# Kernel optimization log

Hardware: AMD Instinct MI355X
Metric: run time of the kernel (lower is better)

The kernel has to match this reference:

```python
import jax, jax.numpy as jnp
import numpy as np

N_NODES = 50000
N_EDGES = 1600000
NODE_DIM = 128
EDGE_DIM = 64
HIDDEN = 128
K_HOPS = 2  # DGL TAGConv default k=2


def _uniform(key, shape, fan_in):
    bound = 1.0 / np.sqrt(fan_in)
    return jax.random.uniform(key, shape, jnp.float32, -bound, bound)


def setup_inputs() -> dict:
    key = jax.random.key(0)
    ks = jax.random.split(key, 12)
    d_msg_in = NODE_DIM + EDGE_DIM
    d_c1_in = (HIDDEN + NODE_DIM) * (K_HOPS + 1)
    d_c2_in = HIDDEN * (K_HOPS + 1)
    return {
        "node_fea": jax.random.normal(ks[0], (N_NODES, NODE_DIM), jnp.float32),
        "edge_fea": jax.random.normal(ks[1], (N_EDGES, EDGE_DIM), jnp.float32),
        "src": jax.random.randint(ks[2], (N_EDGES,), 0, N_NODES),
        "dst": jax.random.randint(ks[3], (N_EDGES,), 0, N_NODES),
        "msg_W": _uniform(ks[4], (d_msg_in, HIDDEN), d_msg_in),
        "msg_b": _uniform(ks[5], (HIDDEN,), d_msg_in),
        "W1": _uniform(ks[6], (d_c1_in, HIDDEN), d_c1_in),
        "b1": _uniform(ks[7], (HIDDEN,), d_c1_in),
        "W2": _uniform(ks[8], (d_c2_in, HIDDEN), d_c2_in),
        "b2": _uniform(ks[9], (HIDDEN,), d_c2_in),
        "Wp": _uniform(ks[10], (HIDDEN, 1), HIDDEN),
        "bp": _uniform(ks[11], (1,), HIDDEN),
    }


def reference(node_fea, edge_fea, src, dst, msg_W, msg_b, W1, b1, W2, b2, Wp, bp):
    n = node_fea.shape[0]
    # --- edge message: relu(Linear([src_fea, edge_fea])) then scatter-sum to dst ---
    msg = jax.nn.relu(jnp.concatenate([node_fea[src], edge_fea], axis=1) @ msg_W + msg_b)
    h_neigh = jax.ops.segment_sum(msg, dst, num_segments=n)  # [N, H]

    # --- TAGConv (k=2) symmetric in-degree normalization, DGL-style ---
    deg = jax.ops.segment_sum(jnp.ones((dst.shape[0],), node_fea.dtype), dst, num_segments=n)
    norm = jnp.maximum(deg, 1.0) ** -0.5  # [N]

    def prop(x):  # x: [N, D] -> norm * A^T (norm * x)
        return norm[:, None] * jax.ops.segment_sum((x * norm[:, None])[src], dst, num_segments=n)

    def tagconv(x, W, b):
        h1 = prop(x)
        h2 = prop(h1)
        return jnp.concatenate([x, h1, h2], axis=1) @ W + b

    h = jax.nn.relu(tagconv(jnp.concatenate([node_fea, h_neigh], axis=1), W1, b1))
    h = jax.nn.relu(tagconv(h, W2, b2))

    # --- dgl.mean_nodes (single graph) then predict ---
    hg = jnp.mean(h, axis=0)  # [H]
    return hg @ Wp + bp  # [1]
```

## Files before the change

kernel.cpp:

```cpp
#include <hip/hip_runtime.h>
#include <hip/hip_bf16.h>


typedef __attribute__((ext_vector_type(8))) short short8;
typedef __attribute__((ext_vector_type(4))) float f32x4;
typedef __attribute__((ext_vector_type(4))) unsigned u32x4;
typedef unsigned short ushort_t;

static __device__ __forceinline__ unsigned short f2bf(float x) {
  union { float f; unsigned u; } v{x};
  unsigned r = v.u + 0x7FFF + ((v.u >> 16) & 1);
  return (unsigned short)(r >> 16);
}
static __device__ __forceinline__ float bf2f(unsigned short h) {
  union { unsigned u; float f; } v{(unsigned)h << 16};
  return v.f;
}
static __device__ __forceinline__ float u2f(unsigned u) {
  union { unsigned u; float f; } v{u};
  return v.f;
}
static __device__ __forceinline__ unsigned cvtpk(float a, float b) {
  unsigned r;
  asm("v_cvt_pk_bf16_f32 %0, %1, %2" : "=v"(r) : "v"(a), "v"(b));
  return r;
}

__global__ void k_deg(const int* __restrict__ dst, int* __restrict__ deg, int E) {
  int i = blockIdx.x * blockDim.x + threadIdx.x;
  int stride = gridDim.x * blockDim.x;
  for (; i < E; i += stride) atomicAdd(&deg[dst[i]], 1);
}

__global__ void k_scan(const int* __restrict__ deg, float* __restrict__ norm,
                       int* __restrict__ offs, int* __restrict__ cursor, int N) {
  __shared__ int part[1024];
  const int t = threadIdx.x;
  const int C = (N + 1023) >> 10;
  const int b = t * C, e = min(b + C, N);
  int s = 0;
  for (int i = b; i < e; ++i) s += deg[i];
  part[t] = s;
  __syncthreads();
  for (int ofs = 1; ofs < 1024; ofs <<= 1) {
    int v = (t >= ofs) ? part[t - ofs] : 0;
    __syncthreads();
    part[t] += v;
    __syncthreads();
  }
  int base = (t == 0) ? 0 : part[t - 1];
  for (int i = b; i < e; ++i) {
    offs[i] = base;
    cursor[i] = base;
    int d = deg[i];
    base += d;
    norm[i] = rsqrtf((float)max(d, 1));
  }
  if (t == 0) offs[N] = part[1023];
}

__global__ void k_csr(const int* __restrict__ src, const int* __restrict__ dst,
                      int* __restrict__ cursor, int* __restrict__ csr_srcnode,
                      int* __restrict__ csr_eid, int* __restrict__ pos2node, int E) {
  int i = blockIdx.x * blockDim.x + threadIdx.x;
  int stride = gridDim.x * blockDim.x;
  for (; i < E; i += stride) {
    int d = dst[i];
    int pos = atomicAdd(&cursor[d], 1);
    csr_srcnode[pos] = src[i];
    csr_eid[pos] = i;
    pos2node[pos] = d;
  }
}

__global__ void k_prepW(const float* __restrict__ W, ushort_t* __restrict__ Wf_hi,
                        ushort_t* __restrict__ Wf_lo, int KC) {
  int id = blockIdx.x * 256 + threadIdx.x;
  if (id >= KC * 8192) return;
  int j = id & 7;
  int l = (id >> 3) & 63;
  int rest = id >> 9;
  int ks = rest & 1, nt = (rest >> 1) & 7, kc = rest >> 4;
  int k = kc * 64 + ks * 32 + (l >> 4) * 8 + j;
  int col = nt * 16 + (l & 15);
  float w = W[(size_t)k * 128 + col];
  unsigned short hi = f2bf(w);
  unsigned short lo = f2bf(w - bf2f(hi));
  Wf_hi[id] = hi;
  Wf_lo[id] = lo;
}

static __device__ __forceinline__ void stage_hilo(const float* base, int sq, int sr,
                                                  ushort_t* Xhi, ushort_t* Xlo) {
#pragma unroll
  for (int i2 = 0; i2 < 2; ++i2) {
    const int o = sq * 2 + i2;
    f32x4 a4 = *(const f32x4*)(base + sq * 16 + i2 * 8);
    f32x4 b4 = *(const f32x4*)(base + sq * 16 + i2 * 8 + 4);
    float x[8] = {a4[0], a4[1], a4[2], a4[3], b4[0], b4[1], b4[2], b4[3]};
    u32x4 vh, vl;
#pragma unroll
    for (int j = 0; j < 4; ++j) {
      unsigned hp = cvtpk(x[2 * j], x[2 * j + 1]);
      float h0 = u2f(hp << 16), h1 = u2f(hp & 0xffff0000u);
      vh[j] = hp;
      vl[j] = cvtpk(x[2 * j] - h0, x[2 * j + 1] - h1);
    }
    const int slot = (sr >> 4) * 128 + o * 16 + (sr & 15);
    *(u32x4*)(Xhi + (size_t)slot * 8) = vh;
    *(u32x4*)(Xlo + (size_t)slot * 8) = vl;
  }
}

__global__ __launch_bounds__(256) void k_mm(
    const float* __restrict__ A0, const ushort_t* __restrict__ Wf_hi,
    const ushort_t* __restrict__ Wf_lo, const float* __restrict__ bias,
    ushort_t* __restrict__ outZ, int M, int KC) {
  __shared__ __align__(16) char lds[49152];
  ushort_t* Xhi = (ushort_t*)lds;
  ushort_t* Xlo = (ushort_t*)(lds + 8192);
  ushort_t* Whi = (ushort_t*)(lds + 16384);
  ushort_t* Wlo = (ushort_t*)(lds + 32768);

  const int t = threadIdx.x;
  const int m0 = blockIdx.x * 64;
  const int l = t & 63, mt = t >> 6;
  const int sr = t & 63, sq = t >> 6;
  const int row = min(m0 + sr, M - 1);

  f32x4 acc[8];
#pragma unroll
  for (int nt = 0; nt < 8; ++nt) acc[nt] = (f32x4){0.f, 0.f, 0.f, 0.f};

  for (int kc = 0; kc < KC; ++kc) {
    __syncthreads();
    {
      const ulong2* gh = (const ulong2*)(Wf_hi + (size_t)kc * 8192);
      const ulong2* gl = (const ulong2*)(Wf_lo + (size_t)kc * 8192);
#pragma unroll
      for (int i = 0; i < 4; ++i) {
        ((ulong2*)Whi)[i * 256 + t] = gh[i * 256 + t];
        ((ulong2*)Wlo)[i * 256 + t] = gl[i * 256 + t];
      }
    }
    stage_hilo(A0 + (size_t)row * 128 + kc * 64, sq, sr, Xhi, Xlo);
    __syncthreads();
    const short8* Xh8 = (const short8*)Xhi;
    const short8* Xl8 = (const short8*)Xlo;
    const short8* Wh8 = (const short8*)Whi;
    const short8* Wl8 = (const short8*)Wlo;
#pragma unroll
    for (int ks = 0; ks < 2; ++ks) {
      short8 ah = Xh8[mt * 128 + ks * 64 + l];
      short8 al = Xl8[mt * 128 + ks * 64 + l];
#pragma unroll
      for (int nt = 0; nt < 8; ++nt) {
        short8 bh = Wh8[(nt * 2 + ks) * 64 + l];
        short8 bl = Wl8[(nt * 2 + ks) * 64 + l];
        acc[nt] = __builtin_amdgcn_mfma_f32_16x16x32_bf16(ah, bh, acc[nt], 0, 0, 0);
        acc[nt] = __builtin_amdgcn_mfma_f32_16x16x32_bf16(al, bh, acc[nt], 0, 0, 0);
        acc[nt] = __builtin_amdgcn_mfma_f32_16x16x32_bf16(ah, bl, acc[nt], 0, 0, 0);
      }
    }
  }
  const int l15 = l & 15, lh = l >> 4;
#pragma unroll
  for (int nt = 0; nt < 8; ++nt) {
    const int col = nt * 16 + l15;
#pragma unroll
    for (int rg = 0; rg < 4; ++rg) {
      const int r = m0 + mt * 16 + lh * 4 + rg;
      if (r < M) outZ[(size_t)r * 128 + col] = f2bf(acc[nt][rg] + bias[col]);
    }
  }
}

template <int BF16A>
__global__ __launch_bounds__(256) void k_mm3(
    const void* __restrict__ A0v, const float* __restrict__ A1, int split64,
    const ushort_t* __restrict__ Wf_hi, const ushort_t* __restrict__ Wf_lo,
    const float* __restrict__ rowscale, float* __restrict__ outA,
    ushort_t* __restrict__ outYB, ushort_t* __restrict__ outYC, int M, int KC) {
  __shared__ __align__(16) char lds[49152];
  ushort_t* Xhi = (ushort_t*)lds;
  ushort_t* Xlo = (ushort_t*)(lds + 8192);
  ushort_t* Whi = (ushort_t*)(lds + 16384);
  ushort_t* Wlo = (ushort_t*)(lds + 32768);

  const int t = threadIdx.x;
  const int m0 = blockIdx.x * 64;
  const int l = t & 63, mt = t >> 6;
  const int sr = t & 63, sq = t >> 6;
  const int row = min(m0 + sr, M - 1);

  f32x4 acc[3][8];
#pragma unroll
  for (int s = 0; s < 3; ++s)
#pragma unroll
    for (int nt = 0; nt < 8; ++nt) acc[s][nt] = (f32x4){0.f, 0.f, 0.f, 0.f};

  for (int kc = 0; kc < KC; ++kc) {
    __syncthreads();
    if constexpr (BF16A) {
      const ushort_t* base = (const ushort_t*)A0v + (size_t)row * 128 + kc * 64;
#pragma unroll
      for (int i2 = 0; i2 < 2; ++i2) {
        const int o = sq * 2 + i2;
        short8 v = *(const short8*)(base + sq * 16 + i2 * 8);
        const int slot = (sr >> 4) * 128 + o * 16 + (sr & 15);
        *(short8*)(Xhi + (size_t)slot * 8) = v;
      }
    } else {
      const float* A0 = (const float*)A0v;
      const float* base = (kc < split64) ? (A0 + (size_t)row * 128 + kc * 64)
                                         : (A1 + (size_t)row * 128 + (kc - split64) * 64);
      stage_hilo(base, sq, sr, Xhi, Xlo);
    }
#pragma unroll
    for (int s = 0; s < 3; ++s) {
      if (s) __syncthreads();
      {
        const ulong2* gh = (const ulong2*)(Wf_hi + ((size_t)s * KC + kc) * 8192);
        const ulong2* gl = (const ulong2*)(Wf_lo + ((size_t)s * KC + kc) * 8192);
#pragma unroll
        for (int i = 0; i < 4; ++i) {
          ((ulong2*)Whi)[i * 256 + t] = gh[i * 256 + t];
          ((ulong2*)Wlo)[i * 256 + t] = gl[i * 256 + t];
        }
      }
      __syncthreads();
      const short8* Xh8 = (const short8*)Xhi;
      const short8* Xl8 = (const short8*)Xlo;
      const short8* Wh8 = (const short8*)Whi;
      const short8* Wl8 = (const short8*)Wlo;
#pragma unroll
      for (int ks = 0; ks < 2; ++ks) {
        short8 ah = Xh8[mt * 128 + ks * 64 + l];
        short8 al;
        if constexpr (!BF16A) al = Xl8[mt * 128 + ks * 64 + l];
#pragma unroll
        for (int nt = 0; nt < 8; ++nt) {
          short8 bh = Wh8[(nt * 2 + ks) * 64 + l];
          short8 bl = Wl8[(nt * 2 + ks) * 64 + l];
          acc[s][nt] = __builtin_amdgcn_mfma_f32_16x16x32_bf16(ah, bh, acc[s][nt], 0, 0, 0);
          if constexpr (!BF16A)
            acc[s][nt] = __builtin_amdgcn_mfma_f32_16x16x32_bf16(al, bh, acc[s][nt], 0, 0, 0);
          acc[s][nt] = __builtin_amdgcn_mfma_f32_16x16x32_bf16(ah, bl, acc[s][nt], 0, 0, 0);
        }
      }
    }
  }
  const int l15 = l & 15, lh = l >> 4;
#pragma unroll
  for (int rg = 0; rg < 4; ++rg) {
    const int r = m0 + mt * 16 + lh * 4 + rg;
    if (r < M) {
      const float rs = rowscale[r];
#pragma unroll
      for (int nt = 0; nt < 8; ++nt) {
        const int col = nt * 16 + l15;
        outA[(size_t)r * 128 + col] = acc[0][nt][rg];
        outYB[(size_t)r * 128 + col] = f2bf(acc[1][nt][rg] * rs);
        outYC[(size_t)r * 128 + col] = f2bf(acc[2][nt][rg] * rs);
      }
    }
  }
}

__global__ __launch_bounds__(512, 6) void k_edge(
    const float* __restrict__ ef, const int* __restrict__ csr_srcnode,
    const int* __restrict__ csr_eid, const int* __restrict__ pos2node,
    const ushort_t* __restrict__ WfB_hi, const ushort_t* __restrict__ WfB_lo,
    const ushort_t* __restrict__ Zb, float* __restrict__ h_neigh) {
  __shared__ __align__(16) char lds[49152];
  ushort_t* Xh = (ushort_t*)lds;
  ushort_t* Whi = (ushort_t*)(lds + 16384);
  ushort_t* Wlo = (ushort_t*)(lds + 32768);
  ushort_t* Cs = (ushort_t*)lds;
  int* sN = (int*)(lds + 32768);

  const int t = threadIdx.x;
  const int b0 = blockIdx.x * 128;
  const int l = t & 63, mt = t >> 6;
  const int col = t & 127, q = t >> 7;
  const int rbase = b0 + q * 32;

  unsigned zp[16];
#pragma unroll
  for (int i = 0; i < 16; ++i) {
    unsigned a = Zb[(size_t)csr_srcnode[rbase + 2 * i] * 128 + col];
    unsigned b = Zb[(size_t)csr_srcnode[rbase + 2 * i + 1] * 128 + col];
    zp[i] = a | (b << 16);
  }
  {
    const ulong2* gh = (const ulong2*)WfB_hi;
    const ulong2* gl = (const ulong2*)WfB_lo;
#pragma unroll
    for (int i = 0; i < 2; ++i) {
      ((ulong2*)Whi)[i * 512 + t] = gh[i * 512 + t];
      ((ulong2*)Wlo)[i * 512 + t] = gl[i * 512 + t];
    }
  }
  {
    const int row = t >> 2, part = t & 3;
    const int eid = csr_eid[b0 + row];
    const float* rowp = ef + (size_t)eid * 64 + part * 16;
#pragma unroll
    for (int i2 = 0; i2 < 2; ++i2) {
      const int o = part * 2 + i2;
      f32x4 a4 = __builtin_nontemporal_load((const f32x4*)(rowp + i2 * 8));
      f32x4 b4 = __builtin_nontemporal_load((const f32x4*)(rowp + i2 * 8 + 4));
      u32x4 vh;
      vh[0] = cvtpk(a4[0], a4[1]);
      vh[1] = cvtpk(a4[2], a4[3]);
      vh[2] = cvtpk(b4[0], b4[1]);
      vh[3] = cvtpk(b4[2], b4[3]);
      const int slot = (row >> 4) * 128 + o * 16 + (row & 15);
      *(u32x4*)(Xh + (size_t)slot * 8) = vh;
    }
  }
  __syncthreads();

  f32x4 acc[8];
#pragma unroll
  for (int nt = 0; nt < 8; ++nt) acc[nt] = (f32x4){0.f, 0.f, 0.f, 0.f};
  {
    const short8* Xh8 = (const short8*)Xh;
    const short8* Wh8 = (const short8*)Whi;
    const short8* Wl8 = (const short8*)Wlo;
#pragma unroll
    for (int ks = 0; ks < 2; ++ks) {
      short8 ah = Xh8[mt * 128 + ks * 64 + l];
#pragma unroll
      for (int nt = 0; nt < 8; ++nt) {
        short8 bh = Wh8[(nt * 2 + ks) * 64 + l];
        short8 bl = Wl8[(nt * 2 + ks) * 64 + l];
        acc[nt] = __builtin_amdgcn_mfma_f32_16x16x32_bf16(ah, bh, acc[nt], 0, 0, 0);
        acc[nt] = __builtin_amdgcn_mfma_f32_16x16x32_bf16(ah, bl, acc[nt], 0, 0, 0);
      }
    }
  }
  __syncthreads();
  if (t < 128) sN[t] = pos2node[b0 + t];
  const int l15 = l & 15, lh = l >> 4;
#pragma unroll
  for (int nt = 0; nt < 8; ++nt) {
#pragma unroll
    for (int rg = 0; rg < 4; ++rg) {
      const int row = mt * 16 + lh * 4 + rg;
      const int c = nt * 16 + l15;
      Cs[row * 128 + (c ^ (((row >> 2) & 3) << 4))] = f2bf(acc[nt][rg]);
    }
  }
  __syncthreads();
  {
    int node = sN[q * 32];
    float ssum = 0.f;
#pragma unroll
    for (int r = 0; r < 32; ++r) {
      const int rr = q * 32 + r;
      float cz = bf2f(Cs[rr * 128 + (col ^ (((rr >> 2) & 3) << 4))]);
      float zf = u2f((r & 1) ? (zp[r >> 1] & 0xffff0000u) : (zp[r >> 1] << 16));
      float v = fmaxf(cz + zf, 0.f);
      if (r == 0) {
        ssum = v;
      } else {
        int n2 = sN[rr];
        if (n2 == node) {
          ssum += v;
        } else {
          unsafeAtomicAdd(&h_neigh[(size_t)node * 128 + col], ssum);
          node = n2;
          ssum = v;
        }
      }
    }
    unsafeAtomicAdd(&h_neigh[(size_t)node * 128 + col], ssum);
  }
}

__global__ __launch_bounds__(256) void k_propA(
    const ushort_t* __restrict__ YCt, const ushort_t* __restrict__ YBt,
    const int* __restrict__ offs, const int* __restrict__ csr_src,
    const float* __restrict__ norm, ushort_t* __restrict__ Qt, int N) {
  const int v = blockIdx.x * 4 + (threadIdx.x >> 6);
  const int lane = threadIdx.x & 63;
  if (v >= N) return;
  const int b = offs[v], e = offs[v + 1];
  const unsigned* yc = (const unsigned*)YCt;
  float ax = 0.f, ay = 0.f;
#pragma unroll 4
  for (int i = b; i < e; ++i) {
    unsigned x = yc[(size_t)csr_src[i] * 64 + lane];
    ax += u2f(x << 16);
    ay += u2f(x & 0xffff0000u);
  }
  float n = norm[v];
  float n2 = n * n;
  unsigned yb = ((const unsigned*)YBt)[(size_t)v * 64 + lane];
  float qx = u2f(yb << 16) + n2 * ax;
  float qy = u2f(yb & 0xffff0000u) + n2 * ay;
  ((unsigned*)Qt)[(size_t)v * 64 + lane] = cvtpk(qx, qy);
}

__global__ __launch_bounds__(256) void k_propB(
    const ushort_t* __restrict__ Qt, const float* __restrict__ YA,
    const float* __restrict__ bias, const int* __restrict__ offs,
    const int* __restrict__ csr_src, const float* __restrict__ norm,
    ushort_t* __restrict__ H, int N) {
  const int v = blockIdx.x * 4 + (threadIdx.x >> 6);
  const int lane = threadIdx.x & 63;
  if (v >= N) return;
  const int b = offs[v], e = offs[v + 1];
  const unsigned* qp = (const unsigned*)Qt;
  float ax = 0.f, ay = 0.f;
#pragma unroll 4
  for (int i = b; i < e; ++i) {
    unsigned x = qp[(size_t)csr_src[i] * 64 + lane];
    ax += u2f(x << 16);
    ay += u2f(x & 0xffff0000u);
  }
  float n = norm[v];
  float2 ya = ((const float2*)YA)[(size_t)v * 64 + lane];
  float2 bb = ((const float2*)bias)[lane];
  float hx = fmaxf(ya.x + n * ax + bb.x, 0.f);
  float hy = fmaxf(ya.y + n * ay + bb.y, 0.f);
  ((unsigned*)H)[(size_t)v * 64 + lane] = cvtpk(hx, hy);
}

__global__ void k_colsum(const ushort_t* __restrict__ h, float* __restrict__ hg, int N) {
  const int t = threadIdx.x;
  const int per = (N + gridDim.x - 1) / gridDim.x;
  const int n0 = blockIdx.x * per, n1 = min(n0 + per, N);
  float s = 0.f;
  for (int n = n0; n < n1; ++n) s += bf2f(h[(size_t)n * 128 + t]);
  unsafeAtomicAdd(&hg[t], s);
}

__global__ void k_final(const float* __restrict__ hg, const float* __restrict__ Wp,
                        const float* __restrict__ bp, float* __restrict__ out,
                        float invN) {
  __shared__ float red[128];
  const int t = threadIdx.x;
  red[t] = hg[t] * invN * Wp[t];
  __syncthreads();
  for (int s = 64; s > 0; s >>= 1) {
    if (t < s) red[t] += red[t + s];
    __syncthreads();
  }
  if (t == 0) out[0] = red[0] + bp[0];
}

extern "C" void kernel_launch(void* const* d_in, const int* in_sizes, int n_in,
                              void* d_out, int out_size, void* d_ws, size_t ws_size,
                              hipStream_t stream) {
  const float* node_fea = (const float*)d_in[0];
  const float* edge_fea = (const float*)d_in[1];
  const int* src = (const int*)d_in[2];
  const int* dst = (const int*)d_in[3];
  const float* msg_W = (const float*)d_in[4];
  const float* msg_b = (const float*)d_in[5];
  const float* W1 = (const float*)d_in[6];
  const float* b1 = (const float*)d_in[7];
  const float* W2 = (const float*)d_in[8];
  const float* b2 = (const float*)d_in[9];
  const float* Wp = (const float*)d_in[10];
  const float* bp = (const float*)d_in[11];

  const int N = in_sizes[0] / 128;
  const int E = in_sizes[2];

  char* p = (char*)d_ws;
  auto alloc = [&](size_t bytes) {
    char* r = p;
    p += (bytes + 255) & ~(size_t)255;
    return r;
  };
  int* deg = (int*)alloc((size_t)N * 4);
  float* norm = (float*)alloc((size_t)N * 4);
  int* offs = (int*)alloc((size_t)(N + 1) * 4);
  int* cursor = (int*)alloc((size_t)N * 4);
  int* csr_srcnode = (int*)alloc((size_t)E * 4);
  int* csr_eid = (int*)alloc((size_t)E * 4);
  int* pos2node = (int*)alloc((size_t)E * 4);
  ushort_t* WfT_hi = (ushort_t*)alloc(2 * 8192 * 2);
  ushort_t* WfT_lo = (ushort_t*)alloc(2 * 8192 * 2);
  ushort_t* WfB_hi = (ushort_t*)alloc(1 * 8192 * 2);
  ushort_t* WfB_lo = (ushort_t*)alloc(1 * 8192 * 2);
  ushort_t* Wf1_hi = (ushort_t*)alloc(3 * 4 * 8192 * 2);
  ushort_t* Wf1_lo = (ushort_t*)alloc(3 * 4 * 8192 * 2);
  ushort_t* Wf2_hi = (ushort_t*)alloc(3 * 2 * 8192 * 2);
  ushort_t* Wf2_lo = (ushort_t*)alloc(3 * 2 * 8192 * 2);
  ushort_t* Zb = (ushort_t*)alloc((size_t)N * 128 * 2);
  float* YA = (float*)alloc((size_t)N * 128 * 4);
  float* hn = (float*)alloc((size_t)N * 128 * 4);
  ushort_t* YBt = (ushort_t*)alloc((size_t)N * 128 * 2);
  ushort_t* YCt = (ushort_t*)alloc((size_t)N * 128 * 2);
  ushort_t* Qt = (ushort_t*)alloc((size_t)N * 128 * 2);
  ushort_t* H1 = (ushort_t*)alloc((size_t)N * 128 * 2);
  ushort_t* H2 = (ushort_t*)alloc((size_t)N * 128 * 2);
  float* hg = (float*)alloc(128 * 4);

  hipMemsetAsync(deg, 0, (size_t)N * 4, stream);
  hipMemsetAsync(hn, 0, (size_t)N * 128 * 4, stream);
  hipMemsetAsync(hg, 0, 128 * 4, stream);

  k_deg<<<2048, 256, 0, stream>>>(dst, deg, E);
  k_scan<<<1, 1024, 0, stream>>>(deg, norm, offs, cursor, N);
  k_csr<<<2048, 256, 0, stream>>>(src, dst, cursor, csr_srcnode, csr_eid, pos2node, E);

  k_prepW<<<64, 256, 0, stream>>>(msg_W, WfT_hi, WfT_lo, 2);
  k_prepW<<<32, 256, 0, stream>>>(msg_W + 128 * 128, WfB_hi, WfB_lo, 1);
  for (int s = 0; s < 3; ++s) {
    k_prepW<<<128, 256, 0, stream>>>(W1 + (size_t)s * 256 * 128,
                                     Wf1_hi + (size_t)s * 4 * 8192,
                                     Wf1_lo + (size_t)s * 4 * 8192, 4);
    k_prepW<<<64, 256, 0, stream>>>(W2 + (size_t)s * 128 * 128,
                                    Wf2_hi + (size_t)s * 2 * 8192,
                                    Wf2_lo + (size_t)s * 2 * 8192, 2);
  }

  const int MB = (N + 63) / 64;
  const int PB = (N + 3) / 4;

  k_mm<<<MB, 256, 0, stream>>>(node_fea, WfT_hi, WfT_lo, msg_b, Zb, N, 2);
  k_edge<<<E / 128, 512, 0, stream>>>(edge_fea, csr_srcnode, csr_eid, pos2node,
                                      WfB_hi, WfB_lo, Zb, hn);

  k_mm3<0><<<MB, 256, 0, stream>>>(node_fea, hn, 2, Wf1_hi, Wf1_lo, norm, YA,
                                   YBt, YCt, N, 4);
  k_propA<<<PB, 256, 0, stream>>>(YCt, YBt, offs, csr_srcnode, norm, Qt, N);
  k_propB<<<PB, 256, 0, stream>>>(Qt, YA, b1, offs, csr_srcnode, norm, H1, N);

  k_mm3<1><<<MB, 256, 0, stream>>>(H1, nullptr, 0, Wf2_hi, Wf2_lo, norm, YA,
                                   YBt, YCt, N, 2);
  k_propA<<<PB, 256, 0, stream>>>(YCt, YBt, offs, csr_srcnode, norm, Qt, N);
  k_propB<<<PB, 256, 0, stream>>>(Qt, YA, b2, offs, csr_srcnode, norm, H2, N);

  k_colsum<<<256, 128, 0, stream>>>(H2, hg, N);
  k_final<<<1, 128, 0, stream>>>(hg, Wp, bp, (float*)d_out, 1.0f / (float)N);
}
```

Measured before the change: 988.4 us.

## Drop LDS staging in GEMMs, widen edge kernel, merge weight prep, unroll gathers

The node GEMM kernels now load A fragments and pre-swizzled weights straight from global memory into registers, removing the LDS staging and block barriers. The edge kernel moves to 1024-thread blocks with 16 rows per thread group, and each wave handles half of the output columns. The eight weight-prep launches become one kernel, and the propagation gathers use four independent accumulators to expose more memory-level parallelism. The trade-off is more redundant global and L2 weight reads per wave, in exchange for fewer launches and less synchronization.

Result: slower. 1.016 ms (+2.8%).

```diff
diff --git a/kernel.cpp b/kernel.cpp
--- a/kernel.cpp
+++ b/kernel.cpp
@@ -73,97 +73,100 @@
   }
 }
 
-__global__ void k_prepW(const float* __restrict__ W, ushort_t* __restrict__ Wf_hi,
-                        ushort_t* __restrict__ Wf_lo, int KC) {
+__global__ void k_prepAll(const float* __restrict__ msg_W, const float* __restrict__ W1,
+                          const float* __restrict__ W2, ushort_t* __restrict__ WfT_hi,
+                          ushort_t* __restrict__ WfT_lo, ushort_t* __restrict__ WfB_hi,
+                          ushort_t* __restrict__ WfB_lo, ushort_t* __restrict__ Wf1_hi,
+                          ushort_t* __restrict__ Wf1_lo, ushort_t* __restrict__ Wf2_hi,
+                          ushort_t* __restrict__ Wf2_lo) {
   int id = blockIdx.x * 256 + threadIdx.x;
-  if (id >= KC * 8192) return;
-  int j = id & 7;
-  int l = (id >> 3) & 63;
-  int rest = id >> 9;
+  const float* W;
+  ushort_t *dh, *dl;
+  int lid;
+  if (id < 16384) {
+    W = msg_W; dh = WfT_hi; dl = WfT_lo; lid = id;
+  } else if (id < 24576) {
+    W = msg_W + 128 * 128; dh = WfB_hi; dl = WfB_lo; lid = id - 16384;
+  } else if (id < 122880) {
+    int sub = id - 24576;
+    int s = sub >> 15;
+    lid = sub & 32767;
+    W = W1 + (size_t)s * 256 * 128;
+    dh = Wf1_hi + (size_t)s * 32768;
+    dl = Wf1_lo + (size_t)s * 32768;
+  } else if (id < 172032) {
+    int sub = id - 122880;
+    int s = sub >> 14;
+    lid = sub & 16383;
+    W = W2 + (size_t)s * 128 * 128;
+    dh = Wf2_hi + (size_t)s * 16384;
+    dl = Wf2_lo + (size_t)s * 16384;
+  } else {
+    return;
+  }
+  int j = lid & 7;
+  int l = (lid >> 3) & 63;
+  int rest = lid >> 9;
   int ks = rest & 1, nt = (rest >> 1) & 7, kc = rest >> 4;
   int k = kc * 64 + ks * 32 + (l >> 4) * 8 + j;
   int col = nt * 16 + (l & 15);
   float w = W[(size_t)k * 128 + col];
   unsigned short hi = f2bf(w);
   unsigned short lo = f2bf(w - bf2f(hi));
-  Wf_hi[id] = hi;
-  Wf_lo[id] = lo;
-}
-
-static __device__ __forceinline__ void stage_hilo(const float* base, int sq, int sr,
-                                                  ushort_t* Xhi, ushort_t* Xlo) {
-#pragma unroll
-  for (int i2 = 0; i2 < 2; ++i2) {
-    const int o = sq * 2 + i2;
-    f32x4 a4 = *(const f32x4*)(base + sq * 16 + i2 * 8);
-    f32x4 b4 = *(const f32x4*)(base + sq * 16 + i2 * 8 + 4);
-    float x[8] = {a4[0], a4[1], a4[2], a4[3], b4[0], b4[1], b4[2], b4[3]};
-    u32x4 vh, vl;
-#pragma unroll
-    for (int j = 0; j < 4; ++j) {
-      unsigned hp = cvtpk(x[2 * j], x[2 * j + 1]);
-      float h0 = u2f(hp << 16), h1 = u2f(hp & 0xffff0000u);
-      vh[j] = hp;
-      vl[j] = cvtpk(x[2 * j] - h0, x[2 * j + 1] - h1);
-    }
-    const int slot = (sr >> 4) * 128 + o * 16 + (sr & 15);
-    *(u32x4*)(Xhi + (size_t)slot * 8) = vh;
-    *(u32x4*)(Xlo + (size_t)slot * 8) = vl;
-  }
+  dh[lid] = hi;
+  dl[lid] = lo;
+}
+
+static __device__ __forceinline__ void load_hilo(const float* p, short8& ah, short8& al) {
+  f32x4 x0 = *(const f32x4*)p;
+  f32x4 x1 = *(const f32x4*)(p + 4);
+  unsigned h0 = cvtpk(x0[0], x0[1]);
+  unsigned h1 = cvtpk(x0[2], x0[3]);
+  unsigned h2 = cvtpk(x1[0], x1[1]);
+  unsigned h3 = cvtpk(x1[2], x1[3]);
+  u32x4 vh = {h0, h1, h2, h3};
+  u32x4 vl = {cvtpk(x0[0] - u2f(h0 << 16), x0[1] - u2f(h0 & 0xffff0000u)),
+              cvtpk(x0[2] - u2f(h1 << 16), x0[3] - u2f(h1 & 0xffff0000u)),
+              cvtpk(x1[0] - u2f(h2 << 16), x1[1] - u2f(h2 & 0xffff0000u)),
+              cvtpk(x1[2] - u2f(h3 << 16), x1[3] - u2f(h3 & 0xffff0000u))};
+  ah = __builtin_bit_cast(short8, vh);
+  al = __builtin_bit_cast(short8, vl);
 }
 
 __global__ __launch_bounds__(256) void k_mm(
     const float* __restrict__ A0, const ushort_t* __restrict__ Wf_hi,
     const ushort_t* __restrict__ Wf_lo, const float* __restrict__ bias,
     ushort_t* __restrict__ outZ, int M, int KC) {
-  __shared__ __align__(16) char lds[49152];
-  ushort_t* Xhi = (ushort_t*)lds;
-  ushort_t* Xlo = (ushort_t*)(lds + 8192);
-  ushort_t* Whi = (ushort_t*)(lds + 16384);
-  ushort_t* Wlo = (ushort_t*)(lds + 32768);
-
   const int t = threadIdx.x;
   const int m0 = blockIdx.x * 64;
   const int l = t & 63, mt = t >> 6;
-  const int sr = t & 63, sq = t >> 6;
-  const int row = min(m0 + sr, M - 1);
+  const int l15 = l & 15, lo4 = l >> 4;
+  const int ar = min(m0 + mt * 16 + l15, M - 1);
 
   f32x4 acc[8];
 #pragma unroll
   for (int nt = 0; nt < 8; ++nt) acc[nt] = (f32x4){0.f, 0.f, 0.f, 0.f};
 
   for (int kc = 0; kc < KC; ++kc) {
-    __syncthreads();
-    {
-      const ulong2* gh = (const ulong2*)(Wf_hi + (size_t)kc * 8192);
-      const ulong2* gl = (const ulong2*)(Wf_lo + (size_t)kc * 8192);
-#pragma unroll
-      for (int i = 0; i < 4; ++i) {
-        ((ulong2*)Whi)[i * 256 + t] = gh[i * 256 + t];
-        ((ulong2*)Wlo)[i * 256 + t] = gl[i * 256 + t];
+    short8 ah[2], al[2];
+#pragma unroll
+    for (int ks = 0; ks < 2; ++ks)
+      load_hilo(A0 + (size_t)ar * 128 + kc * 64 + ks * 32 + lo4 * 8, ah[ks], al[ks]);
+    const short8* wh = (const short8*)(Wf_hi + (size_t)kc * 8192);
+    const short8* wl = (const short8*)(Wf_lo + (size_t)kc * 8192);
+#pragma unroll
+    for (int ks = 0; ks < 2; ++ks) {
+#pragma unroll
+      for (int nt = 0; nt < 8; ++nt) {
+        short8 bh = wh[(nt * 2 + ks) * 64 + l];
+        short8 bl = wl[(nt * 2 + ks) * 64 + l];
+        acc[nt] = __builtin_amdgcn_mfma_f32_16x16x32_bf16(ah[ks], bh, acc[nt], 0, 0, 0);
+        acc[nt] = __builtin_amdgcn_mfma_f32_16x16x32_bf16(al[ks], bh, acc[nt], 0, 0, 0);
+        acc[nt] = __builtin_amdgcn_mfma_f32_16x16x32_bf16(ah[ks], bl, acc[nt], 0, 0, 0);
       }
     }
-    stage_hilo(A0 + (size_t)row * 128 + kc * 64, sq, sr, Xhi, Xlo);
-    __syncthreads();
-    const short8* Xh8 = (const short8*)Xhi;
-    const short8* Xl8 = (const short8*)Xlo;
-    const short8* Wh8 = (const short8*)Whi;
-    const short8* Wl8 = (const short8*)Wlo;
-#pragma unroll
-    for (int ks = 0; ks < 2; ++ks) {
-      short8 ah = Xh8[mt * 128 + ks * 64 + l];
-      short8 al = Xl8[mt * 128 + ks * 64 + l];
-#pragma unroll
-      for (int nt = 0; nt < 8; ++nt) {
-        short8 bh = Wh8[(nt * 2 + ks) * 64 + l];
-        short8 bl = Wl8[(nt * 2 + ks) * 64 + l];
-        acc[nt] = __builtin_amdgcn_mfma_f32_16x16x32_bf16(ah, bh, acc[nt], 0, 0, 0);
-        acc[nt] = __builtin_amdgcn_mfma_f32_16x16x32_bf16(al, bh, acc[nt], 0, 0, 0);
-        acc[nt] = __builtin_amdgcn_mfma_f32_16x16x32_bf16(ah, bl, acc[nt], 0, 0, 0);
-      }
-    }
-  }
-  const int l15 = l & 15, lh = l >> 4;
+  }
+  const int lh = lo4;
 #pragma unroll
   for (int nt = 0; nt < 8; ++nt) {
     const int col = nt * 16 + l15;
@@ -181,17 +184,11 @@
     const ushort_t* __restrict__ Wf_hi, const ushort_t* __restrict__ Wf_lo,
     const float* __restrict__ rowscale, float* __restrict__ outA,
     ushort_t* __restrict__ outYB, ushort_t* __restrict__ outYC, int M, int KC) {
-  __shared__ __align__(16) char lds[49152];
-  ushort_t* Xhi = (ushort_t*)lds;
-  ushort_t* Xlo = (ushort_t*)(lds + 8192);
-  ushort_t* Whi = (ushort_t*)(lds + 16384);
-  ushort_t* Wlo = (ushort_t*)(lds + 32768);
-
   const int t = threadIdx.x;
   const int m0 = blockIdx.x * 64;
   const int l = t & 63, mt = t >> 6;
-  const int sr = t & 63, sq = t >> 6;
-  const int row = min(m0 + sr, M - 1);
+  const int l15 = l & 15, lo4 = l >> 4;
+  const int ar = min(m0 + mt * 16 + l15, M - 1);
 
   f32x4 acc[3][8];
 #pragma unroll
@@ -200,57 +197,38 @@
     for (int nt = 0; nt < 8; ++nt) acc[s][nt] = (f32x4){0.f, 0.f, 0.f, 0.f};
 
   for (int kc = 0; kc < KC; ++kc) {
-    __syncthreads();
+    short8 ah[2], al[2];
     if constexpr (BF16A) {
-      const ushort_t* base = (const ushort_t*)A0v + (size_t)row * 128 + kc * 64;
-#pragma unroll
-      for (int i2 = 0; i2 < 2; ++i2) {
-        const int o = sq * 2 + i2;
-        short8 v = *(const short8*)(base + sq * 16 + i2 * 8);
-        const int slot = (sr >> 4) * 128 + o * 16 + (sr & 15);
-        *(short8*)(Xhi + (size_t)slot * 8) = v;
-      }
+      const ushort_t* base = (const ushort_t*)A0v + (size_t)ar * 128 + kc * 64 + lo4 * 8;
+      ah[0] = *(const short8*)base;
+      ah[1] = *(const short8*)(base + 32);
     } else {
       const float* A0 = (const float*)A0v;
-      const float* base = (kc < split64) ? (A0 + (size_t)row * 128 + kc * 64)
-                                         : (A1 + (size_t)row * 128 + (kc - split64) * 64);
-      stage_hilo(base, sq, sr, Xhi, Xlo);
+      const float* base = (kc < split64) ? (A0 + (size_t)ar * 128 + kc * 64)
+                                         : (A1 + (size_t)ar * 128 + (kc - split64) * 64);
+#pragma unroll
+      for (int ks = 0; ks < 2; ++ks)
+        load_hilo(base + ks * 32 + lo4 * 8, ah[ks], al[ks]);
     }
 #pragma unroll
     for (int s = 0; s < 3; ++s) {
-      if (s) __syncthreads();
-      {
-        const ulong2* gh = (const ulong2*)(Wf_hi + ((size_t)s * KC + kc) * 8192);
-        const ulong2* gl = (const ulong2*)(Wf_lo + ((size_t)s * KC + kc) * 8192);
-#pragma unroll
-        for (int i = 0; i < 4; ++i) {
-          ((ulong2*)Whi)[i * 256 + t] = gh[i * 256 + t];
-          ((ulong2*)Wlo)[i * 256 + t] = gl[i * 256 + t];
+      const short8* wh = (const short8*)(Wf_hi + ((size_t)s * KC + kc) * 8192);
+      const short8* wl = (const short8*)(Wf_lo + ((size_t)s * KC + kc) * 8192);
+#pragma unroll
+      for (int ks = 0; ks < 2; ++ks) {
+#pragma unroll
+        for (int nt = 0; nt < 8; ++nt) {
+          short8 bh = wh[(nt * 2 + ks) * 64 + l];
+          short8 bl = wl[(nt * 2 + ks) * 64 + l];
+          acc[s][nt] = __builtin_amdgcn_mfma_f32_16x16x32_bf16(ah[ks], bh, acc[s][nt], 0, 0, 0);
+          if constexpr (!BF16A)
+            acc[s][nt] = __builtin_amdgcn_mfma_f32_16x16x32_bf16(al[ks], bh, acc[s][nt], 0, 0, 0);
+          acc[s][nt] = __builtin_amdgcn_mfma_f32_16x16x32_bf16(ah[ks], bl, acc[s][nt], 0, 0, 0);
         }
       }
-      __syncthreads();
-      const short8* Xh8 = (const short8*)Xhi;
-      const short8* Xl8 = (const short8*)Xlo;
-      const short8* Wh8 = (const short8*)Whi;
-      const short8* Wl8 = (const short8*)Wlo;
-#pragma unroll
-      for (int ks = 0; ks < 2; ++ks) {
-        short8 ah = Xh8[mt * 128 + ks * 64 + l];
-        short8 al;
-        if constexpr (!BF16A) al = Xl8[mt * 128 + ks * 64 + l];
-#pragma unroll
-        for (int nt = 0; nt < 8; ++nt) {
-          short8 bh = Wh8[(nt * 2 + ks) * 64 + l];
-          short8 bl = Wl8[(nt * 2 + ks) * 64 + l];
-          acc[s][nt] = __builtin_amdgcn_mfma_f32_16x16x32_bf16(ah, bh, acc[s][nt], 0, 0, 0);
-          if constexpr (!BF16A)
-            acc[s][nt] = __builtin_amdgcn_mfma_f32_16x16x32_bf16(al, bh, acc[s][nt], 0, 0, 0);
-          acc[s][nt] = __builtin_amdgcn_mfma_f32_16x16x32_bf16(ah, bl, acc[s][nt], 0, 0, 0);
-        }
-      }
-    }
-  }
-  const int l15 = l & 15, lh = l >> 4;
+    }
+  }
+  const int lh = lo4;
 #pragma unroll
   for (int rg = 0; rg < 4; ++rg) {
     const int r = m0 + mt * 16 + lh * 4 + rg;
@@ -267,7 +245,7 @@
   }
 }
 
-__global__ __launch_bounds__(512, 6) void k_edge(
+__global__ __launch_bounds__(1024, 8) void k_edge(
     const float* __restrict__ ef, const int* __restrict__ csr_srcnode,
     const int* __restrict__ csr_eid, const int* __restrict__ pos2node,
     const ushort_t* __restrict__ WfB_hi, const ushort_t* __restrict__ WfB_lo,
@@ -281,49 +259,39 @@
 
   const int t = threadIdx.x;
   const int b0 = blockIdx.x * 128;
-  const int l = t & 63, mt = t >> 6;
-  const int col = t & 127, q = t >> 7;
-  const int rbase = b0 + q * 32;
-
-  unsigned zp[16];
-#pragma unroll
-  for (int i = 0; i < 16; ++i) {
+  const int l = t & 63, w = t >> 6;
+  const int mt = w >> 1, nh = w & 1;
+  const int col = t & 127, g = t >> 7;
+  const int rbase = b0 + g * 16;
+
+  unsigned zp[8];
+#pragma unroll
+  for (int i = 0; i < 8; ++i) {
     unsigned a = Zb[(size_t)csr_srcnode[rbase + 2 * i] * 128 + col];
     unsigned b = Zb[(size_t)csr_srcnode[rbase + 2 * i + 1] * 128 + col];
     zp[i] = a | (b << 16);
   }
+  ((ulong2*)Whi)[t] = ((const ulong2*)WfB_hi)[t];
+  ((ulong2*)Wlo)[t] = ((const ulong2*)WfB_lo)[t];
   {
-    const ulong2* gh = (const ulong2*)WfB_hi;
-    const ulong2* gl = (const ulong2*)WfB_lo;
-#pragma unroll
-    for (int i = 0; i < 2; ++i) {
-      ((ulong2*)Whi)[i * 512 + t] = gh[i * 512 + t];
-      ((ulong2*)Wlo)[i * 512 + t] = gl[i * 512 + t];
-    }
-  }
-  {
-    const int row = t >> 2, part = t & 3;
+    const int row = t >> 3, part = t & 7;
     const int eid = csr_eid[b0 + row];
-    const float* rowp = ef + (size_t)eid * 64 + part * 16;
-#pragma unroll
-    for (int i2 = 0; i2 < 2; ++i2) {
-      const int o = part * 2 + i2;
-      f32x4 a4 = __builtin_nontemporal_load((const f32x4*)(rowp + i2 * 8));
-      f32x4 b4 = __builtin_nontemporal_load((const f32x4*)(rowp + i2 * 8 + 4));
-      u32x4 vh;
-      vh[0] = cvtpk(a4[0], a4[1]);
-      vh[1] = cvtpk(a4[2], a4[3]);
-      vh[2] = cvtpk(b4[0], b4[1]);
-      vh[3] = cvtpk(b4[2], b4[3]);
-      const int slot = (row >> 4) * 128 + o * 16 + (row & 15);
-      *(u32x4*)(Xh + (size_t)slot * 8) = vh;
-    }
+    const float* rowp = ef + (size_t)eid * 64 + part * 8;
+    f32x4 a4 = __builtin_nontemporal_load((const f32x4*)rowp);
+    f32x4 b4 = __builtin_nontemporal_load((const f32x4*)(rowp + 4));
+    u32x4 vh;
+    vh[0] = cvtpk(a4[0], a4[1]);
+    vh[1] = cvtpk(a4[2], a4[3]);
+    vh[2] = cvtpk(b4[0], b4[1]);
+    vh[3] = cvtpk(b4[2], b4[3]);
+    const int slot = (row >> 4) * 128 + part * 16 + (row & 15);
+    *(u32x4*)(Xh + (size_t)slot * 8) = vh;
   }
   __syncthreads();
 
-  f32x4 acc[8];
-#pragma unroll
-  for (int nt = 0; nt < 8; ++nt) acc[nt] = (f32x4){0.f, 0.f, 0.f, 0.f};
+  f32x4 acc[4];
+#pragma unroll
+  for (int nt = 0; nt < 4; ++nt) acc[nt] = (f32x4){0.f, 0.f, 0.f, 0.f};
   {
     const short8* Xh8 = (const short8*)Xh;
     const short8* Wh8 = (const short8*)Whi;
@@ -332,9 +300,10 @@
     for (int ks = 0; ks < 2; ++ks) {
       short8 ah = Xh8[mt * 128 + ks * 64 + l];
 #pragma unroll
-      for (int nt = 0; nt < 8; ++nt) {
-        short8 bh = Wh8[(nt * 2 + ks) * 64 + l];
-        short8 bl = Wl8[(nt * 2 + ks) * 64 + l];
+      for (int nt = 0; nt < 4; ++nt) {
+        const int ntg = nh * 4 + nt;
+        short8 bh = Wh8[(ntg * 2 + ks) * 64 + l];
+        short8 bl = Wl8[(ntg * 2 + ks) * 64 + l];
         acc[nt] = __builtin_amdgcn_mfma_f32_16x16x32_bf16(ah, bh, acc[nt], 0, 0, 0);
         acc[nt] = __builtin_amdgcn_mfma_f32_16x16x32_bf16(ah, bl, acc[nt], 0, 0, 0);
       }
@@ -344,21 +313,21 @@
   if (t < 128) sN[t] = pos2node[b0 + t];
   const int l15 = l & 15, lh = l >> 4;
 #pragma unroll
-  for (int nt = 0; nt < 8; ++nt) {
+  for (int nt = 0; nt < 4; ++nt) {
 #pragma unroll
     for (int rg = 0; rg < 4; ++rg) {
       const int row = mt * 16 + lh * 4 + rg;
-      const int c = nt * 16 + l15;
+      const int c = nh * 64 + nt * 16 + l15;
       Cs[row * 128 + (c ^ (((row >> 2) & 3) << 4))] = f2bf(acc[nt][rg]);
     }
   }
   __syncthreads();
   {
-    int node = sN[q * 32];
+    int node = sN[g * 16];
     float ssum = 0.f;
 #pragma unroll
-    for (int r = 0; r < 32; ++r) {
-      const int rr = q * 32 + r;
+    for (int r = 0; r < 16; ++r) {
+      const int rr = g * 16 + r;
       float cz = bf2f(Cs[rr * 128 + (col ^ (((rr >> 2) & 3) << 4))]);
       float zf = u2f((r & 1) ? (zp[r >> 1] & 0xffff0000u) : (zp[r >> 1] << 16));
       float v = fmaxf(cz + zf, 0.f);
@@ -388,19 +357,33 @@
   if (v >= N) return;
   const int b = offs[v], e = offs[v + 1];
   const unsigned* yc = (const unsigned*)YCt;
-  float ax = 0.f, ay = 0.f;
-#pragma unroll 4
-  for (int i = b; i < e; ++i) {
-    unsigned x = yc[(size_t)csr_src[i] * 64 + lane];
-    ax += u2f(x << 16);
-    ay += u2f(x & 0xffff0000u);
-  }
-  float n = norm[v];
-  float n2 = n * n;
-  unsigned yb = ((const unsigned*)YBt)[(size_t)v * 64 + lane];
-  float qx = u2f(yb << 16) + n2 * ax;
-  float qy = u2f(yb & 0xffff0000u) + n2 * ay;
-  ((unsigned*)Qt)[(size_t)v * 64 + lane] = cvtpk(qx, qy);
+  float ax0 = 0.f, ay0 = 0.f, ax1 = 0.f, ay1 = 0.f;
+  float ax2 = 0.f, ay2 = 0.f, ax3 = 0.f, ay3 = 0.f;
+  int i = b;
+  const int e4 = b + ((e - b) & ~3);
+  for (; i < e4; i += 4) {
+    const int s0 = csr_src[i], s1 = csr_src[i + 1];
+    const int s2 = csr_src[i + 2], s3 = csr_src[i + 3];
+    const unsigned x0 = yc[(size_t)s0 * 64 + lane];
+    const unsigned x1 = yc[(size_t)s1 * 64 + lane];
+    const unsigned x2 = yc[(size_t)s2 * 64 + lane];
+    const unsigned x3 = yc[(size_t)s3 * 64 + lane];
+    ax0 += u2f(x0 << 16); ay0 += u2f(x0 & 0xffff0000u);
+    ax1 += u2f(x1 << 16); ay1 += u2f(x1 & 0xffff0000u);
+    ax2 += u2f(x2 << 16); ay2 += u2f(x2 & 0xffff0000u);
+    ax3 += u2f(x3 << 16); ay3 += u2f(x3 & 0xffff0000u);
+  }
+  for (; i < e; ++i) {
+    const unsigned x = yc[(size_t)csr_src[i] * 64 + lane];
+    ax0 += u2f(x << 16); ay0 += u2f(x & 0xffff0000u);
+  }
+  const float ax = (ax0 + ax1) + (ax2 + ax3);
+  const float ay = (ay0 + ay1) + (ay2 + ay3);
+  const float n = norm[v];
+  const float n2 = n * n;
+  const unsigned yb = ((const unsigned*)YBt)[(size_t)v * 64 + lane];
+  ((unsigned*)Qt)[(size_t)v * 64 + lane] =
+      cvtpk(u2f(yb << 16) + n2 * ax, u2f(yb & 0xffff0000u) + n2 * ay);
 }
 
 __global__ __launch_bounds__(256) void k_propB(
@@ -413,18 +396,33 @@
   if (v >= N) return;
   const int b = offs[v], e = offs[v + 1];
   const unsigned* qp = (const unsigned*)Qt;
-  float ax = 0.f, ay = 0.f;
-#pragma unroll 4
-  for (int i = b; i < e; ++i) {
-    unsigned x = qp[(size_t)csr_src[i] * 64 + lane];
-    ax += u2f(x << 16);
-    ay += u2f(x & 0xffff0000u);
-  }
-  float n = norm[v];
-  float2 ya = ((const float2*)YA)[(size_t)v * 64 + lane];
-  float2 bb = ((const float2*)bias)[lane];
-  float hx = fmaxf(ya.x + n * ax + bb.x, 0.f);
-  float hy = fmaxf(ya.y + n * ay + bb.y, 0.f);
+  float ax0 = 0.f, ay0 = 0.f, ax1 = 0.f, ay1 = 0.f;
+  float ax2 = 0.f, ay2 = 0.f, ax3 = 0.f, ay3 = 0.f;
+  int i = b;
+  const int e4 = b + ((e - b) & ~3);
+  for (; i < e4; i += 4) {
+    const int s0 = csr_src[i], s1 = csr_src[i + 1];
+    const int s2 = csr_src[i + 2], s3 = csr_src[i + 3];
+    const unsigned x0 = qp[(size_t)s0 * 64 + lane];
+    const unsigned x1 = qp[(size_t)s1 * 64 + lane];
+    const unsigned x2 = qp[(size_t)s2 * 64 + lane];
+    const unsigned x3 = qp[(size_t)s3 * 64 + lane];
+    ax0 += u2f(x0 << 16); ay0 += u2f(x0 & 0xffff0000u);
+    ax1 += u2f(x1 << 16); ay1 += u2f(x1 & 0xffff0000u);
+    ax2 += u2f(x2 << 16); ay2 += u2f(x2 & 0xffff0000u);
+    ax3 += u2f(x3 << 16); ay3 += u2f(x3 & 0xffff0000u);
+  }
+  for (; i < e; ++i) {
+    const unsigned x = qp[(size_t)csr_src[i] * 64 + lane];
+    ax0 += u2f(x << 16); ay0 += u2f(x & 0xffff0000u);
+  }
+  const float ax = (ax0 + ax1) + (ax2 + ax3);
+  const float ay = (ay0 + ay1) + (ay2 + ay3);
+  const float n = norm[v];
+  const float2 ya = ((const float2*)YA)[(size_t)v * 64 + lane];
+  const float2 bb = ((const float2*)bias)[lane];
+  const float hx = fmaxf(ya.x + n * ax + bb.x, 0.f);
+  const float hy = fmaxf(ya.y + n * ay + bb.y, 0.f);
   ((unsigned*)H)[(size_t)v * 64 + lane] = cvtpk(hx, hy);
 }
 
@@ -508,24 +506,15 @@
   k_deg<<<2048, 256, 0, stream>>>(dst, deg, E);
   k_scan<<<1, 1024, 0, stream>>>(deg, norm, offs, cursor, N);
   k_csr<<<2048, 256, 0, stream>>>(src, dst, cursor, csr_srcnode, csr_eid, pos2node, E);
-
-  k_prepW<<<64, 256, 0, stream>>>(msg_W, WfT_hi, WfT_lo, 2);
-  k_prepW<<<32, 256, 0, stream>>>(msg_W + 128 * 128, WfB_hi, WfB_lo, 1);
-  for (int s = 0; s < 3; ++s) {
-    k_prepW<<<128, 256, 0, stream>>>(W1 + (size_t)s * 256 * 128,
-                                     Wf1_hi + (size_t)s * 4 * 8192,
-                                     Wf1_lo + (size_t)s * 4 * 8192, 4);
-    k_prepW<<<64, 256, 0, stream>>>(W2 + (size_t)s * 128 * 128,
-                                    Wf2_hi + (size_t)s * 2 * 8192,
-                                    Wf2_lo + (size_t)s * 2 * 8192, 2);
-  }
+  k_prepAll<<<672, 256, 0, stream>>>(msg_W, W1, W2, WfT_hi, WfT_lo, WfB_hi, WfB_lo,
+                                     Wf1_hi, Wf1_lo, Wf2_hi, Wf2_lo);
 
   const int MB = (N + 63) / 64;
   const int PB = (N + 3) / 4;
 
   k_mm<<<MB, 256, 0, stream>>>(node_fea, WfT_hi, WfT_lo, msg_b, Zb, N, 2);
-  k_edge<<<E / 128, 512, 0, stream>>>(edge_fea, csr_srcnode, csr_eid, pos2node,
-                                      WfB_hi, WfB_lo, Zb, hn);
+  k_edge<<<E / 128, 1024, 0, stream>>>(edge_fea, csr_srcnode, csr_eid, pos2node,
+                                       WfB_hi, WfB_lo, Zb, hn);
 
   k_mm3<0><<<MB, 256, 0, stream>>>(node_fea, hn, 2, Wf1_hi, Wf1_lo, norm, YA,
                                    YBt, YCt, N, 4);
```
